# Kernel optimization log

Measured on AMD Instinct MI355X. Metric: run time of the kernel, lower is better.

## Reference

```python
import jax, jax.numpy as jnp
import numpy as np

D_MODEL = 1024
NUM_HEADS = 16
HEAD_DIM = D_MODEL // NUM_HEADS
B, S = 2, 2048


def setup_inputs() -> dict:
    key = jax.random.key(0)
    ks = jax.random.split(key, 9)
    scale = 1.0 / np.sqrt(D_MODEL)
    return {
        "x": jax.random.normal(ks[0], (B, S, D_MODEL), jnp.float32),
        "y": jax.random.normal(ks[1], (B, S, D_MODEL), jnp.float32),
        "mask": jnp.zeros((B, S, S), jnp.float32),
        "Wkv": jax.random.normal(ks[2], (D_MODEL, 2 * D_MODEL), jnp.float32) * scale,
        "bkv": jnp.zeros((2 * D_MODEL,), jnp.float32),
        "Wq": jax.random.normal(ks[3], (D_MODEL, D_MODEL), jnp.float32) * scale,
        "bq": jnp.zeros((D_MODEL,), jnp.float32),
        "Wo": jax.random.normal(ks[4], (D_MODEL, D_MODEL), jnp.float32) * scale,
        "bo": jnp.zeros((D_MODEL,), jnp.float32),
    }


def reference(x, y, mask, Wkv, bkv, Wq, bq, Wo, bo):
    b, s, d = x.shape
    h, hd = NUM_HEADS, HEAD_DIM
    # projections
    kv = x @ Wkv + bkv                       # [B, S, 2D]
    q = y @ Wq + bq                          # [B, S, D]
    kv = kv.reshape(b, s, h, 2 * hd).transpose(0, 2, 1, 3)  # [B, H, S, 2hd]
    q = q.reshape(b, s, h, hd).transpose(0, 2, 1, 3)        # [B, H, S, hd]
    k, v = kv[..., :hd], kv[..., hd:]
    # scaled dot-product attention with additive per-batch mask
    scaled = jnp.einsum("bhqd,bhkd->bhqk", q, k) / jnp.sqrt(jnp.float32(hd))
    scaled = scaled + mask[:, None, :, :]    # mask [B,S,S] broadcast over heads
    attn = jax.nn.softmax(scaled, axis=-1)
    vals = jnp.einsum("bhqk,bhkd->bhqd", attn, v)            # [B, H, S, hd]
    vals = vals.transpose(0, 2, 1, 3).reshape(b, s, d)       # [B, S, D]
    return vals @ Wo + bo
```

## Files before the change

kernel.cpp:

```cpp
#include <hip/hip_runtime.h>
#include <hip/hip_bf16.h>

#define D_MODEL 1024
#define NHEADS 16
#define HD 64
#define BATCH 2
#define SEQ 2048
#define BS (BATCH*SEQ)

typedef __bf16 bf16;
typedef bf16 bf16x4 __attribute__((ext_vector_type(4)));
typedef bf16 bf16x8 __attribute__((ext_vector_type(8)));
typedef float f32x4 __attribute__((ext_vector_type(4)));

#define AS1 __attribute__((address_space(1)))
#define AS3 __attribute__((address_space(3)))

__device__ __forceinline__ void gload_lds16(const void* g, void* l) {
  __builtin_amdgcn_global_load_lds((AS1 const unsigned int*)g, (AS3 unsigned int*)l, 16, 0, 0);
}

__device__ __forceinline__ float exp2_fast(float x) {
#if __has_builtin(__builtin_amdgcn_exp2f)
  return __builtin_amdgcn_exp2f(x);
#else
  float r;
  asm("v_exp_f32 %0, %1\n\ts_nop 1" : "=v"(r) : "v"(x));
  return r;
#endif
}

__global__ __launch_bounds__(256)
void prep_kernel(const float* __restrict__ x, const float* __restrict__ y,
                 const float* __restrict__ mask,
                 const float* __restrict__ Wkv, const float* __restrict__ Wq,
                 const float* __restrict__ Wo,
                 bf16* __restrict__ xb, bf16* __restrict__ yb,
                 bf16* __restrict__ Wkvt, bf16* __restrict__ Wqt,
                 bf16* __restrict__ Wot, int* __restrict__ flag) {
  __shared__ bf16 tile[64][72];
  const int blk = blockIdx.x;
  const int t = threadIdx.x;

  if (blk < 4096) {
    const float* in = (blk < 2048) ? x : y;
    bf16* out = (blk < 2048) ? xb : yb;
    int i = (blk & 2047) * 256 + t;
    const float4* p = (const float4*)(in + (size_t)i * 8);
    float4 a = p[0], b = p[1];
    bf16x8 o;
    o[0]=(bf16)a.x; o[1]=(bf16)a.y; o[2]=(bf16)a.z; o[3]=(bf16)a.w;
    o[4]=(bf16)b.x; o[5]=(bf16)b.y; o[6]=(bf16)b.z; o[7]=(bf16)b.w;
    *(bf16x8*)(out + (size_t)i * 8) = o;
  } else if (blk < 5120) {
    const float* tin; bf16* tout; int C, tt;
    if (blk < 4608)      { tin = Wkv; tout = Wkvt; C = 2048; tt = blk - 4096; }
    else if (blk < 4864) { tin = Wq;  tout = Wqt;  C = 1024; tt = blk - 4608; }
    else                 { tin = Wo;  tout = Wot;  C = 1024; tt = blk - 4864; }
    const int R = 1024;
    const int r0 = (tt & 15) * 64;
    const int c0 = (tt >> 4) * 64;
    {
      int r = t >> 2, cc = (t & 3) * 16;
      const float* src = tin + (size_t)(r0 + r) * C + c0 + cc;
      #pragma unroll
      for (int j = 0; j < 16; j += 4) {
        float4 v = *(const float4*)(src + j);
        tile[r][cc + j + 0] = (bf16)v.x;
        tile[r][cc + j + 1] = (bf16)v.y;
        tile[r][cc + j + 2] = (bf16)v.z;
        tile[r][cc + j + 3] = (bf16)v.w;
      }
    }
    __syncthreads();
    {
      int c = t >> 2, rr = (t & 3) * 16;
      bf16* dst = tout + (size_t)(c0 + c) * R + r0 + rr;
      bf16x8 o0, o1;
      #pragma unroll
      for (int j = 0; j < 8; j++) { o0[j] = tile[rr + j][c]; o1[j] = tile[rr + 8 + j][c]; }
      *(bf16x8*)dst = o0;
      *(bf16x8*)(dst + 8) = o1;
    }
  } else {
    const int n4 = BATCH * SEQ * SEQ / 4;
    int i = (blk - 5120) * 256 + t;
    const int stride = 1024 * 256;
    int any = 0;
    for (; i < n4; i += stride) {
      float4 v = *(const float4*)(mask + (size_t)i * 4);
      if (v.x != 0.f || v.y != 0.f || v.z != 0.f || v.w != 0.f) any = 1;
    }
    if (__ballot(any) && (t & 63) == 0) atomicOr(flag, 1);
  }
}

__global__ __launch_bounds__(256)
void qkv_gemm(const bf16* __restrict__ xb, const bf16* __restrict__ yb,
              const bf16* __restrict__ Wkvt, const bf16* __restrict__ Wqt,
              const float* __restrict__ bkv, const float* __restrict__ bq,
              bf16* __restrict__ KVb, bf16* __restrict__ Qbuf,
              bf16* __restrict__ Vt, float QSCL) {
  __shared__ char lds[32768];
  char* Alds = lds;
  char* Blds = lds + 16384;
  const int K = 1024;
  const int t = threadIdx.x;
  const int lane = t & 63;
  const int wid = t >> 6;
  const int m0 = blockIdx.x * 128;
  const int by = blockIdx.y;
  const bool isQ = by >= 16;
  const int n0 = (isQ ? by - 16 : by) * 128;
  const bf16* A = isQ ? yb : xb;
  const bf16* Bt = isQ ? Wqt : Wkvt;
  const int wr = wid >> 1, wc = wid & 1;

  f32x4 acc[4][4] = {};

  int rowL[4], colL[4];
  #pragma unroll
  for (int i = 0; i < 4; i++) {
    int L = t * 16 + i * 4096;
    int r = L >> 7;
    rowL[i] = r;
    colL[i] = (L & 127) ^ ((r & 7) << 4);
  }
  const char* Ab = (const char*)A;
  const char* Bb = (const char*)Bt;
  const size_t rs = (size_t)K * 2;

  for (int k0 = 0; k0 < K; k0 += 64) {
    #pragma unroll
    for (int i = 0; i < 4; i++) {
      gload_lds16(Ab + (size_t)(m0 + rowL[i]) * rs + (size_t)k0 * 2 + colL[i],
                  Alds + i * 4096 + t * 16);
      gload_lds16(Bb + (size_t)(n0 + rowL[i]) * rs + (size_t)k0 * 2 + colL[i],
                  Blds + i * 4096 + t * 16);
    }
    __syncthreads();
    #pragma unroll
    for (int kb = 0; kb < 2; kb++) {
      bf16x8 af[4], bfr[4];
      #pragma unroll
      for (int m = 0; m < 4; m++) {
        int r = wr * 64 + m * 16 + (lane & 15);
        int cb = (kb * 64 + ((lane >> 4) << 4)) ^ ((r & 7) << 4);
        af[m] = *(const bf16x8*)(Alds + r * 128 + cb);
      }
      #pragma unroll
      for (int n = 0; n < 4; n++) {
        int r = wc * 64 + n * 16 + (lane & 15);
        int cb = (kb * 64 + ((lane >> 4) << 4)) ^ ((r & 7) << 4);
        bfr[n] = *(const bf16x8*)(Blds + r * 128 + cb);
      }
      #pragma unroll
      for (int m = 0; m < 4; m++)
        #pragma unroll
        for (int n = 0; n < 4; n++)
          acc[m][n] = __builtin_amdgcn_mfma_f32_16x16x32_bf16(af[m], bfr[n], acc[m][n], 0, 0, 0);
    }
    __syncthreads();
  }

  if (!isQ && wc == 1) {
    const int h = n0 >> 7;
    const int bb = m0 >> 11;
    #pragma unroll
    for (int n = 0; n < 4; n++) {
      const int d = n * 16 + (lane & 15);
      const float bv = bkv[n0 + 64 + d];
      bf16* vrow = Vt + ((size_t)((bb * NHEADS + h) * HD + d)) * SEQ;
      #pragma unroll
      for (int m = 0; m < 4; m++) {
        const int rb = m0 + wr * 64 + m * 16 + ((lane >> 4) << 2);
        const int s = rb & (SEQ - 1);
        bf16x4 v;
        #pragma unroll
        for (int j = 0; j < 4; j++) v[j] = (bf16)(acc[m][n][j] + bv);
        *(bf16x4*)(vrow + s) = v;
      }
    }
  } else if (!isQ) {
    #pragma unroll
    for (int m = 0; m < 4; m++) {
      const int rb = m0 + wr * 64 + m * 16 + ((lane >> 4) << 2);
      #pragma unroll
      for (int n = 0; n < 4; n++) {
        const int cg = n0 + n * 16 + (lane & 15);
        const float bv = bkv[cg];
        #pragma unroll
        for (int j = 0; j < 4; j++)
          KVb[(size_t)(rb + j) * 2048 + cg] = (bf16)(acc[m][n][j] + bv);
      }
    }
  } else {
    #pragma unroll
    for (int m = 0; m < 4; m++) {
      const int rb = m0 + wr * 64 + m * 16 + ((lane >> 4) << 2);
      #pragma unroll
      for (int n = 0; n < 4; n++) {
        const int cg = n0 + wc * 64 + n * 16 + (lane & 15);
        const float bv = bq[cg];
        #pragma unroll
        for (int j = 0; j < 4; j++)
          Qbuf[(size_t)(rb + j) * 1024 + cg] = (bf16)((acc[m][n][j] + bv) * QSCL);
      }
    }
  }
}

__global__ __launch_bounds__(256)
void gemm_o(const bf16* __restrict__ A, const bf16* __restrict__ Bt,
            const float* __restrict__ bias, float* __restrict__ C,
            int M, int N, int K) {
  __shared__ char lds[32768];
  char* Alds = lds;
  char* Blds = lds + 16384;
  const int t = threadIdx.x;
  const int lane = t & 63;
  const int wid = t >> 6;
  const int m0 = blockIdx.x * 128;
  const int n0 = blockIdx.y * 128;
  const int wr = wid >> 1, wc = wid & 1;

  f32x4 acc[4][4] = {};

  int rowL[4], colL[4];
  #pragma unroll
  for (int i = 0; i < 4; i++) {
    int L = t * 16 + i * 4096;
    int r = L >> 7;
    rowL[i] = r;
    colL[i] = (L & 127) ^ ((r & 7) << 4);
  }
  const char* Ab = (const char*)A;
  const char* Bb = (const char*)Bt;
  const size_t rs = (size_t)K * 2;

  for (int k0 = 0; k0 < K; k0 += 64) {
    #pragma unroll
    for (int i = 0; i < 4; i++) {
      gload_lds16(Ab + (size_t)(m0 + rowL[i]) * rs + (size_t)k0 * 2 + colL[i],
                  Alds + i * 4096 + t * 16);
      gload_lds16(Bb + (size_t)(n0 + rowL[i]) * rs + (size_t)k0 * 2 + colL[i],
                  Blds + i * 4096 + t * 16);
    }
    __syncthreads();
    #pragma unroll
    for (int kb = 0; kb < 2; kb++) {
      bf16x8 af[4], bfr[4];
      #pragma unroll
      for (int m = 0; m < 4; m++) {
        int r = wr * 64 + m * 16 + (lane & 15);
        int cb = (kb * 64 + ((lane >> 4) << 4)) ^ ((r & 7) << 4);
        af[m] = *(const bf16x8*)(Alds + r * 128 + cb);
      }
      #pragma unroll
      for (int n = 0; n < 4; n++) {
        int r = wc * 64 + n * 16 + (lane & 15);
        int cb = (kb * 64 + ((lane >> 4) << 4)) ^ ((r & 7) << 4);
        bfr[n] = *(const bf16x8*)(Blds + r * 128 + cb);
      }
      #pragma unroll
      for (int m = 0; m < 4; m++)
        #pragma unroll
        for (int n = 0; n < 4; n++)
          acc[m][n] = __builtin_amdgcn_mfma_f32_16x16x32_bf16(af[m], bfr[n], acc[m][n], 0, 0, 0);
    }
    __syncthreads();
  }

  #pragma unroll
  for (int m = 0; m < 4; m++) {
    const int rb = m0 + wr * 64 + m * 16 + ((lane >> 4) << 2);
    #pragma unroll
    for (int n = 0; n < 4; n++) {
      const int cg = n0 + wc * 64 + n * 16 + (lane & 15);
      const float bv = bias[cg];
      #pragma unroll
      for (int j = 0; j < 4; j++)
        C[(size_t)(rb + j) * N + cg] = acc[m][n][j] + bv;
    }
  }
}

__global__ __launch_bounds__(256)
void attn_kernel(const bf16* __restrict__ Qb, const bf16* __restrict__ KV,
                 const bf16* __restrict__ Vt, const float* __restrict__ mask,
                 const int* __restrict__ flag, bf16* __restrict__ vals) {
  __shared__ char lds[49152];
  const int t = threadIdx.x;
  const int lane = t & 63;
  const int wid = t >> 6;
  const int g = lane >> 4;
  const int lq = lane & 15;
  char* Pw = lds + 32768 + wid * 4096;

  int wg = ((blockIdx.x & 7) << 6) | (blockIdx.x >> 3);
  const int qt = wg & 15;
  const int h = (wg >> 4) & 15;
  const int b = wg >> 8;
  const int q0 = qt * 128 + wid * 32;
  const bool use_mask = (*flag) != 0;

  bf16x8 qf[2][2];
  #pragma unroll
  for (int m = 0; m < 2; m++)
    #pragma unroll
    for (int kb = 0; kb < 2; kb++) {
      int r = q0 + m * 16 + lq;
      qf[m][kb] = *(const bf16x8*)(Qb + (size_t)(b * SEQ + r) * D_MODEL + h * HD + kb * 32 + g * 8);
    }

  f32x4 oacc[2][4] = {};
  float mrun[2], lrun[2];
  mrun[0] = mrun[1] = -1e30f;
  lrun[0] = lrun[1] = 0.f;

  int kvOff[2][4];
  #pragma unroll
  for (int kb = 0; kb < 2; kb++)
    #pragma unroll
    for (int n = 0; n < 4; n++) {
      int r = n * 16 + lq;
      kvOff[kb][n] = r * 128 + ((kb * 64 + (g << 4)) ^ ((r & 7) << 4));
    }
  int pROff[2][2];
  #pragma unroll
  for (int m = 0; m < 2; m++)
    #pragma unroll
    for (int kb = 0; kb < 2; kb++) {
      int r = m * 16 + lq;
      pROff[m][kb] = r * 128 + ((kb * 64 + (g << 4)) ^ ((r & 7) << 4));
    }
  int pWOff[2][4];
  #pragma unroll
  for (int m = 0; m < 2; m++) {
    int r = m * 16 + lq;
    int swz = (r & 7) << 4;
    #pragma unroll
    for (int n = 0; n < 4; n++)
      pWOff[m][n] = r * 128 + ((n * 32 + g * 8) ^ swz);
  }

  int rowL[2], colL[2];
  #pragma unroll
  for (int i = 0; i < 2; i++) {
    int L = t * 16 + i * 4096;
    int r = L >> 7;
    rowL[i] = r;
    colL[i] = (L & 127) ^ ((r & 7) << 4);
  }
  const char* KVb = (const char*)KV;
  const char* Vtb = (const char*)Vt;

  auto stage = [&](int kt, int c) {
    const int kv0 = kt * 64;
    char* Kb = lds + c * 16384;
    char* Vb = Kb + 8192;
    #pragma unroll
    for (int i = 0; i < 2; i++) {
      gload_lds16(KVb + (size_t)(b * SEQ + kv0 + rowL[i]) * (2 * D_MODEL * 2) + h * 256 + colL[i],
                  Kb + i * 4096 + t * 16);
      gload_lds16(Vtb + (size_t)((b * NHEADS + h) * HD + rowL[i]) * (SEQ * 2) + kv0 * 2 + colL[i],
                  Vb + i * 4096 + t * 16);
    }
  };

  stage(0, 0);
  __syncthreads();
  int cur = 0;

  const int NT = SEQ / 64;
  for (int kt = 0; kt < NT; kt++) {
    if (kt + 1 < NT) stage(kt + 1, cur ^ 1);
    char* Klds = lds + cur * 16384;
    char* Vlds = Klds + 8192;
    const int kv0 = kt * 64;

    f32x4 sacc[2][4] = {};
    __builtin_amdgcn_s_setprio(1);
    #pragma unroll
    for (int kb = 0; kb < 2; kb++) {
      bf16x8 kf[4];
      #pragma unroll
      for (int n = 0; n < 4; n++)
        kf[n] = *(const bf16x8*)(Klds + kvOff[kb][n]);
      #pragma unroll
      for (int m = 0; m < 2; m++)
        #pragma unroll
        for (int n = 0; n < 4; n++)
          sacc[m][n] = __builtin_amdgcn_mfma_f32_16x16x32_bf16(kf[n], qf[m][kb], sacc[m][n], 0, 0, 0);
    }
    __builtin_amdgcn_s_setprio(0);

    if (use_mask) {
      #pragma unroll
      for (int m = 0; m < 2; m++) {
        int qg = q0 + m * 16 + lq;
        const float* mrow = mask + ((size_t)b * SEQ + qg) * SEQ + kv0;
        #pragma unroll
        for (int n = 0; n < 4; n++)
          #pragma unroll
          for (int j = 0; j < 4; j++)
            sacc[m][n][j] += mrow[n * 16 + g * 4 + j] * 1.44269504f;
      }
    }

    float pm[2];
    #pragma unroll
    for (int m = 0; m < 2; m++) {
      float a0 = fmaxf(fmaxf(sacc[m][0][0], sacc[m][0][1]), fmaxf(sacc[m][0][2], sacc[m][0][3]));
      float a1 = fmaxf(fmaxf(sacc[m][1][0], sacc[m][1][1]), fmaxf(sacc[m][1][2], sacc[m][1][3]));
      float a2 = fmaxf(fmaxf(sacc[m][2][0], sacc[m][2][1]), fmaxf(sacc[m][2][2], sacc[m][2][3]));
      float a3 = fmaxf(fmaxf(sacc[m][3][0], sacc[m][3][1]), fmaxf(sacc[m][3][2], sacc[m][3][3]));
      float v = fmaxf(fmaxf(a0, a1), fmaxf(a2, a3));
      v = fmaxf(v, __shfl_xor(v, 16, 64));
      v = fmaxf(v, __shfl_xor(v, 32, 64));
      pm[m] = v;
    }

    int nogrow = (pm[0] <= mrun[0] + 8.f) && (pm[1] <= mrun[1] + 8.f);
    if (!__all(nogrow)) {
      #pragma unroll
      for (int m = 0; m < 2; m++) {
        float mn = fmaxf(mrun[m], pm[m]);
        float sf = exp2_fast(mrun[m] - mn);
        mrun[m] = mn;
        lrun[m] *= sf;
        float sfj[4];
        #pragma unroll
        for (int j = 0; j < 4; j++) sfj[j] = __shfl(sf, (g << 2) + j, 64);
        #pragma unroll
        for (int n = 0; n < 4; n++)
          #pragma unroll
          for (int j = 0; j < 4; j++)
            oacc[m][n][j] *= sfj[j];
      }
    }

    #pragma unroll
    for (int m = 0; m < 2; m++) {
      float rsn[4];
      #pragma unroll
      for (int n = 0; n < 4; n++) {
        float e0 = exp2_fast(sacc[m][n][0] - mrun[m]);
        float e1 = exp2_fast(sacc[m][n][1] - mrun[m]);
        float e2 = exp2_fast(sacc[m][n][2] - mrun[m]);
        float e3 = exp2_fast(sacc[m][n][3] - mrun[m]);
        rsn[n] = (e0 + e1) + (e2 + e3);
        bf16x4 p = {(bf16)e0, (bf16)e1, (bf16)e2, (bf16)e3};
        *(bf16x4*)(Pw + pWOff[m][n]) = p;
      }
      lrun[m] += (rsn[0] + rsn[1]) + (rsn[2] + rsn[3]);
    }


    __builtin_amdgcn_s_setprio(1);
    #pragma unroll
    for (int kb = 0; kb < 2; kb++) {
      bf16x8 pf[2], vf[4];
      #pragma unroll
      for (int m = 0; m < 2; m++)
        pf[m] = *(const bf16x8*)(Pw + pROff[m][kb]);
      #pragma unroll
      for (int n = 0; n < 4; n++)
        vf[n] = *(const bf16x8*)(Vlds + kvOff[kb][n]);
      #pragma unroll
      for (int m = 0; m < 2; m++)
        #pragma unroll
        for (int n = 0; n < 4; n++)
          oacc[m][n] = __builtin_amdgcn_mfma_f32_16x16x32_bf16(pf[m], vf[n], oacc[m][n], 0, 0, 0);
    }
    __builtin_amdgcn_s_setprio(0);

    __syncthreads();
    cur ^= 1;
  }

  #pragma unroll
  for (int m = 0; m < 2; m++) {
    lrun[m] += __shfl_xor(lrun[m], 16, 64);
    lrun[m] += __shfl_xor(lrun[m], 32, 64);
  }

  #pragma unroll
  for (int m = 0; m < 2; m++) {
    float inv[4];
    #pragma unroll
    for (int j = 0; j < 4; j++)
      inv[j] = 1.f / __shfl(lrun[m], (g << 2) + j, 64);
    #pragma unroll
    for (int n = 0; n < 4; n++) {
      int cg = h * HD + n * 16 + lq;
      #pragma unroll
      for (int j = 0; j < 4; j++) {
        int rg = b * SEQ + q0 + m * 16 + g * 4 + j;
        vals[(size_t)rg * D_MODEL + cg] = (bf16)(oacc[m][n][j] * inv[j]);
      }
    }
  }
}

extern "C" void kernel_launch(void* const* d_in, const int* in_sizes, int n_in,
                              void* d_out, int out_size, void* d_ws, size_t ws_size,
                              hipStream_t stream) {
  const float* x    = (const float*)d_in[0];
  const float* y    = (const float*)d_in[1];
  const float* mask = (const float*)d_in[2];
  const float* Wkv  = (const float*)d_in[3];
  const float* bkv  = (const float*)d_in[4];
  const float* Wq   = (const float*)d_in[5];
  const float* bq   = (const float*)d_in[6];
  const float* Wo   = (const float*)d_in[7];
  const float* bo   = (const float*)d_in[8];
  float* out = (float*)d_out;

  char* ws = (char*)d_ws;
  bf16* xb   = (bf16*)(ws);
  bf16* yb   = (bf16*)(ws + (8ull << 20));
  bf16* Wkvt = (bf16*)(ws + (16ull << 20));
  bf16* Wqt  = (bf16*)(ws + (20ull << 20));
  bf16* Wot  = (bf16*)(ws + (22ull << 20));
  bf16* KVb  = (bf16*)(ws + (24ull << 20));
  bf16* Qbuf = (bf16*)(ws + (40ull << 20));
  bf16* Vt   = (bf16*)(ws + (48ull << 20));
  bf16* vals = (bf16*)(ws + (56ull << 20));
  int*  flag = (int*)(ws + (64ull << 20));

  const float QSCL = 0.125f * 1.44269504f;

  hipMemsetAsync(flag, 0, 4, stream);
  prep_kernel<<<6144, 256, 0, stream>>>(x, y, mask, Wkv, Wq, Wo,
                                        xb, yb, Wkvt, Wqt, Wot, flag);
  qkv_gemm<<<dim3(32, 24), 256, 0, stream>>>(xb, yb, Wkvt, Wqt, bkv, bq,
                                             KVb, Qbuf, Vt, QSCL);
  attn_kernel<<<512, 256, 0, stream>>>(Qbuf, KVb, Vt, mask, flag, vals);
  gemm_o<<<dim3(32, 8), 256, 0, stream>>>(vals, Wot, bo, out, 4096, 1024, 1024);
}
```

Baseline: 144.6 us.

## Split attention over KV halves with merge kernel, compact K buffer, smaller O-GEMM tiles

Attention now runs 1024 workgroups, each covering half of the KV sequence, and writes normalized partial outputs plus per-row max and sum. A new merge kernel combines the two halves using log-sum-exp weights. K is stored compactly, without the interleaved V columns, which halves the row stride for K loads. The output GEMM uses 64-row tiles to double its workgroup count. The aim is better occupancy across the GPU's compute units, at the cost of an extra kernel launch and an extra pass over the partial outputs in memory.

New measurement: 146.6 us. About the same (+1.4%).

```diff
diff --git a/kernel.cpp b/kernel.cpp
--- a/kernel.cpp
+++ b/kernel.cpp
@@ -99,7 +99,7 @@
 void qkv_gemm(const bf16* __restrict__ xb, const bf16* __restrict__ yb,
               const bf16* __restrict__ Wkvt, const bf16* __restrict__ Wqt,
               const float* __restrict__ bkv, const float* __restrict__ bq,
-              bf16* __restrict__ KVb, bf16* __restrict__ Qbuf,
+              bf16* __restrict__ Kc, bf16* __restrict__ Qbuf,
               bf16* __restrict__ Vt, float QSCL) {
   __shared__ char lds[32768];
   char* Alds = lds;
@@ -188,10 +188,11 @@
       #pragma unroll
       for (int n = 0; n < 4; n++) {
         const int cg = n0 + n * 16 + (lane & 15);
+        const int cc = (n0 >> 1) + n * 16 + (lane & 15);
         const float bv = bkv[cg];
         #pragma unroll
         for (int j = 0; j < 4; j++)
-          KVb[(size_t)(rb + j) * 2048 + cg] = (bf16)(acc[m][n][j] + bv);
+          Kc[(size_t)(rb + j) * 1024 + cc] = (bf16)(acc[m][n][j] + bv);
       }
     }
   } else {
@@ -214,17 +215,17 @@
 void gemm_o(const bf16* __restrict__ A, const bf16* __restrict__ Bt,
             const float* __restrict__ bias, float* __restrict__ C,
             int M, int N, int K) {
-  __shared__ char lds[32768];
+  __shared__ char lds[24576];
   char* Alds = lds;
-  char* Blds = lds + 16384;
+  char* Blds = lds + 8192;
   const int t = threadIdx.x;
   const int lane = t & 63;
   const int wid = t >> 6;
-  const int m0 = blockIdx.x * 128;
+  const int m0 = blockIdx.x * 64;
   const int n0 = blockIdx.y * 128;
   const int wr = wid >> 1, wc = wid & 1;
 
-  f32x4 acc[4][4] = {};
+  f32x4 acc[2][4] = {};
 
   int rowL[4], colL[4];
   #pragma unroll
@@ -240,19 +241,20 @@
 
   for (int k0 = 0; k0 < K; k0 += 64) {
     #pragma unroll
-    for (int i = 0; i < 4; i++) {
+    for (int i = 0; i < 2; i++)
       gload_lds16(Ab + (size_t)(m0 + rowL[i]) * rs + (size_t)k0 * 2 + colL[i],
                   Alds + i * 4096 + t * 16);
+    #pragma unroll
+    for (int i = 0; i < 4; i++)
       gload_lds16(Bb + (size_t)(n0 + rowL[i]) * rs + (size_t)k0 * 2 + colL[i],
                   Blds + i * 4096 + t * 16);
-    }
     __syncthreads();
     #pragma unroll
     for (int kb = 0; kb < 2; kb++) {
-      bf16x8 af[4], bfr[4];
-      #pragma unroll
-      for (int m = 0; m < 4; m++) {
-        int r = wr * 64 + m * 16 + (lane & 15);
+      bf16x8 af[2], bfr[4];
+      #pragma unroll
+      for (int m = 0; m < 2; m++) {
+        int r = wr * 32 + m * 16 + (lane & 15);
         int cb = (kb * 64 + ((lane >> 4) << 4)) ^ ((r & 7) << 4);
         af[m] = *(const bf16x8*)(Alds + r * 128 + cb);
       }
@@ -263,7 +265,7 @@
         bfr[n] = *(const bf16x8*)(Blds + r * 128 + cb);
       }
       #pragma unroll
-      for (int m = 0; m < 4; m++)
+      for (int m = 0; m < 2; m++)
         #pragma unroll
         for (int n = 0; n < 4; n++)
           acc[m][n] = __builtin_amdgcn_mfma_f32_16x16x32_bf16(af[m], bfr[n], acc[m][n], 0, 0, 0);
@@ -272,8 +274,8 @@
   }
 
   #pragma unroll
-  for (int m = 0; m < 4; m++) {
-    const int rb = m0 + wr * 64 + m * 16 + ((lane >> 4) << 2);
+  for (int m = 0; m < 2; m++) {
+    const int rb = m0 + wr * 32 + m * 16 + ((lane >> 4) << 2);
     #pragma unroll
     for (int n = 0; n < 4; n++) {
       const int cg = n0 + wc * 64 + n * 16 + (lane & 15);
@@ -286,9 +288,11 @@
 }
 
 __global__ __launch_bounds__(256)
-void attn_kernel(const bf16* __restrict__ Qb, const bf16* __restrict__ KV,
+void attn_kernel(const bf16* __restrict__ Qb, const bf16* __restrict__ Kc,
                  const bf16* __restrict__ Vt, const float* __restrict__ mask,
-                 const int* __restrict__ flag, bf16* __restrict__ vals) {
+                 const int* __restrict__ flag,
+                 bf16* __restrict__ Opart0, bf16* __restrict__ Opart1,
+                 float* __restrict__ ml) {
   __shared__ char lds[49152];
   const int t = threadIdx.x;
   const int lane = t & 63;
@@ -297,10 +301,11 @@
   const int lq = lane & 15;
   char* Pw = lds + 32768 + wid * 4096;
 
-  int wg = ((blockIdx.x & 7) << 6) | (blockIdx.x >> 3);
+  int wg = ((blockIdx.x & 7) << 7) | (blockIdx.x >> 3);
   const int qt = wg & 15;
-  const int h = (wg >> 4) & 15;
-  const int b = wg >> 8;
+  const int s = (wg >> 4) & 1;
+  const int h = (wg >> 5) & 15;
+  const int b = wg >> 9;
   const int q0 = qt * 128 + wid * 32;
   const bool use_mask = (*flag) != 0;
 
@@ -352,29 +357,30 @@
     rowL[i] = r;
     colL[i] = (L & 127) ^ ((r & 7) << 4);
   }
-  const char* KVb = (const char*)KV;
+  const char* Kb = (const char*)Kc;
   const char* Vtb = (const char*)Vt;
 
   auto stage = [&](int kt, int c) {
     const int kv0 = kt * 64;
-    char* Kb = lds + c * 16384;
-    char* Vb = Kb + 8192;
+    char* Kd = lds + c * 16384;
+    char* Vd = Kd + 8192;
     #pragma unroll
     for (int i = 0; i < 2; i++) {
-      gload_lds16(KVb + (size_t)(b * SEQ + kv0 + rowL[i]) * (2 * D_MODEL * 2) + h * 256 + colL[i],
-                  Kb + i * 4096 + t * 16);
+      gload_lds16(Kb + (size_t)(b * SEQ + kv0 + rowL[i]) * 2048 + h * 128 + colL[i],
+                  Kd + i * 4096 + t * 16);
       gload_lds16(Vtb + (size_t)((b * NHEADS + h) * HD + rowL[i]) * (SEQ * 2) + kv0 * 2 + colL[i],
-                  Vb + i * 4096 + t * 16);
+                  Vd + i * 4096 + t * 16);
     }
   };
 
-  stage(0, 0);
+  const int kt0 = s * 16;
+  stage(kt0, 0);
   __syncthreads();
   int cur = 0;
 
-  const int NT = SEQ / 64;
-  for (int kt = 0; kt < NT; kt++) {
-    if (kt + 1 < NT) stage(kt + 1, cur ^ 1);
+  for (int it = 0; it < 16; it++) {
+    const int kt = kt0 + it;
+    if (it + 1 < 16) stage(kt + 1, cur ^ 1);
     char* Klds = lds + cur * 16384;
     char* Vlds = Klds + 8192;
     const int kv0 = kt * 64;
@@ -456,7 +462,6 @@
       lrun[m] += (rsn[0] + rsn[1]) + (rsn[2] + rsn[3]);
     }
 
-
     __builtin_amdgcn_s_setprio(1);
     #pragma unroll
     for (int kb = 0; kb < 2; kb++) {
@@ -485,6 +490,16 @@
     lrun[m] += __shfl_xor(lrun[m], 32, 64);
   }
 
+  if (g == 0) {
+    #pragma unroll
+    for (int m = 0; m < 2; m++) {
+      int q = q0 + m * 16 + lq;
+      float2 v; v.x = mrun[m]; v.y = lrun[m];
+      *(float2*)(ml + (((size_t)(b * SEQ + q)) * NHEADS + h) * 4 + s * 2) = v;
+    }
+  }
+
+  bf16* Op = s ? Opart1 : Opart0;
   #pragma unroll
   for (int m = 0; m < 2; m++) {
     float inv[4];
@@ -497,10 +512,32 @@
       #pragma unroll
       for (int j = 0; j < 4; j++) {
         int rg = b * SEQ + q0 + m * 16 + g * 4 + j;
-        vals[(size_t)rg * D_MODEL + cg] = (bf16)(oacc[m][n][j] * inv[j]);
-      }
-    }
-  }
+        Op[(size_t)rg * D_MODEL + cg] = (bf16)(oacc[m][n][j] * inv[j]);
+      }
+    }
+  }
+}
+
+__global__ __launch_bounds__(256)
+void merge_kernel(const bf16* __restrict__ O0, bf16* __restrict__ O1,
+                  const float* __restrict__ ml) {
+  int e = blockIdx.x * 256 + threadIdx.x;
+  int r = e >> 7;
+  int c0 = (e & 127) * 8;
+  int h = c0 >> 6;
+  const float4 m4 = *(const float4*)(ml + ((size_t)r * NHEADS + h) * 4);
+  float mm = fmaxf(m4.x, m4.z);
+  float w0 = m4.y * exp2_fast(m4.x - mm);
+  float w1 = m4.w * exp2_fast(m4.z - mm);
+  float nrm = 1.f / (w0 + w1);
+  w0 *= nrm; w1 *= nrm;
+  bf16x8 a = *(const bf16x8*)(O0 + (size_t)r * D_MODEL + c0);
+  bf16x8 bb = *(const bf16x8*)(O1 + (size_t)r * D_MODEL + c0);
+  bf16x8 o;
+  #pragma unroll
+  for (int j = 0; j < 8; j++)
+    o[j] = (bf16)((float)a[j] * w0 + (float)bb[j] * w1);
+  *(bf16x8*)(O1 + (size_t)r * D_MODEL + c0) = o;
 }
 
 extern "C" void kernel_launch(void* const* d_in, const int* in_sizes, int n_in,
@@ -518,24 +555,29 @@
   float* out = (float*)d_out;
 
   char* ws = (char*)d_ws;
+  float* ml  = (float*)(ws);
   bf16* xb   = (bf16*)(ws);
   bf16* yb   = (bf16*)(ws + (8ull << 20));
   bf16* Wkvt = (bf16*)(ws + (16ull << 20));
   bf16* Wqt  = (bf16*)(ws + (20ull << 20));
   bf16* Wot  = (bf16*)(ws + (22ull << 20));
-  bf16* KVb  = (bf16*)(ws + (24ull << 20));
+  bf16* Kc   = (bf16*)(ws + (24ull << 20));
+  bf16* Op0  = (bf16*)(ws + (32ull << 20));
   bf16* Qbuf = (bf16*)(ws + (40ull << 20));
   bf16* Vt   = (bf16*)(ws + (48ull << 20));
   bf16* vals = (bf16*)(ws + (56ull << 20));
   int*  flag = (int*)(ws + (64ull << 20));
 
+
   const float QSCL = 0.125f * 1.44269504f;
 
   hipMemsetAsync(flag, 0, 4, stream);
   prep_kernel<<<6144, 256, 0, stream>>>(x, y, mask, Wkv, Wq, Wo,
                                         xb, yb, Wkvt, Wqt, Wot, flag);
   qkv_gemm<<<dim3(32, 24), 256, 0, stream>>>(xb, yb, Wkvt, Wqt, bkv, bq,
-                                             KVb, Qbuf, Vt, QSCL);
-  attn_kernel<<<512, 256, 0, stream>>>(Qbuf, KVb, Vt, mask, flag, vals);
-  gemm_o<<<dim3(32, 8), 256, 0, stream>>>(vals, Wot, bo, out, 4096, 1024, 1024);
-}
+                                             Kc, Qbuf, Vt, QSCL);
+  attn_kernel<<<1024, 256, 0, stream>>>(Qbuf, Kc, Vt, mask, flag,
+                                        Op0, vals, ml);
+  merge_kernel<<<2048, 256, 0, stream>>>(Op0, vals, ml);
+  gemm_o<<<dim3(64, 8), 256, 0, stream>>>(vals, Wot, bo, out, 4096, 1024, 1024);
+}
```
